# Performance work log

Measured on AMD Instinct MI355X. Metric: run time of the kernel, lower is better.

## Reference

```python
import jax, jax.numpy as jnp
import numpy as np

B_, T_, D_ = 2, 2048, 1024
DS_, EXPAND_ = 16, 2
DI_ = D_ * EXPAND_


def setup_inputs() -> dict:
    key = jax.random.key(0)
    ks = jax.random.split(key, 10)
    s = 0.02
    x = jax.random.normal(ks[0], (B_, T_, D_), jnp.float32)
    Win = jax.random.normal(ks[1], (2 * DI_, D_), jnp.float32) * s   # in_proj weight [2di, d]
    A_log = jax.random.uniform(ks[2], (DI_, DS_), jnp.float32, -4.0, -1.0)
    WB = jax.random.normal(ks[3], (DS_, D_), jnp.float32) * s        # B_proj
    WC = jax.random.normal(ks[4], (DS_, D_), jnp.float32) * s        # C_proj
    Wdt = jax.random.normal(ks[5], (DI_, D_), jnp.float32) * s       # dt_proj weight
    bdt = jnp.zeros((DI_,), jnp.float32)                              # dt_proj bias
    dt_bias = jnp.full((DI_,), -4.0, jnp.float32)
    gamma = jnp.ones((DI_,), jnp.float32)
    beta = jnp.zeros((DI_,), jnp.float32)
    Wout = jax.random.normal(ks[6], (D_, DI_), jnp.float32) * s      # out_proj
    return dict(x=x, Win=Win, A_log=A_log, WB=WB, WC=WC, Wdt=Wdt, bdt=bdt,
                dt_bias=dt_bias, gamma=gamma, beta=beta, Wout=Wout)


def _forward(x, Win, A_log, WB, WC, Wdt, bdt, dt_bias, gamma, beta, Wout):
    B, T, d = x.shape
    di, ds = A_log.shape
    xz = jnp.einsum('btd,ed->bte', x, Win)            # [B,T,2di]
    xi, z = xz[..., :di], xz[..., di:]
    z = jax.nn.silu(z)
    A = -jnp.exp(A_log)                                # [di,ds]
    Bm = jnp.einsum('btd,sd->bts', x, WB)              # [B,T,ds]
    C = jnp.einsum('btd,sd->bts', x, WC)               # [B,T,ds]
    dt = jax.nn.softplus(jnp.einsum('btd,ed->bte', x, Wdt) + bdt + dt_bias)  # [B,T,di]
    dtA = dt[..., None] * A                            # [B,T,di,ds]
    denom = 1.0 - dtA * 0.5
    A_bar = (1.0 + dtA * 0.5) / denom                  # bilinear (Tustin)
    B_bar = dt[..., None] / denom                      # [B,T,di,ds]

    def step(state, inp):
        Ab, Bb, Bt, xt, Ct = inp                       # [B,di,ds],[B,di,ds],[B,ds],[B,di],[B,ds]
        state = Ab * state + Bb * Bt[:, None, :] * xt[:, :, None]
        out = jnp.einsum('bds,bs->bd', state, Ct)
        return state, out

    tm = lambda a: jnp.swapaxes(a, 0, 1)               # time-major for scan
    state0 = jnp.zeros((B, di, ds), x.dtype)
    state, outs = jax.lax.scan(step, state0, (tm(A_bar), tm(B_bar), tm(Bm), tm(xi), tm(C)))
    out = jnp.swapaxes(outs, 0, 1) * z                 # [B,T,di]
    mu = out.mean(-1, keepdims=True)
    var = ((out - mu) ** 2).mean(-1, keepdims=True)
    normed = (out - mu) * jax.lax.rsqrt(var + 1e-5) * gamma + beta
    y = jnp.einsum('bte,de->btd', normed, Wout)
    return y, state


def reference(x, Win, A_log, WB, WC, Wdt, bdt, dt_bias, gamma, beta, Wout):
    return _forward(x, Win, A_log, WB, WC, Wdt, bdt, dt_bias, gamma, beta, Wout)
```

## Files before the change

### kernel.cpp

```cpp
#include <hip/hip_runtime.h>
#include <stdint.h>

#define B_ 2
#define T_ 2048
#define D_ 1024
#define DI_ 2048
#define DS_ 16
#define MROWS (B_*T_)
#define NC_ 32
#define CL_ (T_/NC_)
#define TT_ 32

typedef unsigned short u16;
typedef __attribute__((ext_vector_type(4))) float f32x4;
typedef __attribute__((ext_vector_type(8))) short short8;
typedef __attribute__((ext_vector_type(4))) unsigned short u16x4;

__device__ __forceinline__ float bf2f(u16 u) {
    union { uint32_t i; float f; } v; v.i = ((uint32_t)u) << 16; return v.f;
}
__device__ __forceinline__ u16 f2bf(float f) {
    union { float f; uint32_t i; } v; v.f = f;
    uint32_t r = v.i + 0x7fff + ((v.i >> 16) & 1);
    return (u16)(r >> 16);
}

__global__ __launch_bounds__(256) void cvt_kernel(const float* __restrict__ in,
                                                  u16* __restrict__ out, int n4) {
    int i = blockIdx.x * 256 + threadIdx.x;
    if (i < n4) {
        float4 v = ((const float4*)in)[i];
        u16x4 o;
        o.x = f2bf(v.x); o.y = f2bf(v.y); o.z = f2bf(v.z); o.w = f2bf(v.w);
        ((u16x4*)out)[i] = o;
    }
}

__global__ __launch_bounds__(256) void gemm_in(
    const u16* __restrict__ A, const u16* __restrict__ Win,
    const u16* __restrict__ Wdt,
    u16* __restrict__ xi, u16* __restrict__ z, u16* __restrict__ dtout,
    const float* __restrict__ b1, const float* __restrict__ b2) {
    __shared__ u16 lA[2][128 * 32];
    __shared__ u16 lB[2][128 * 32];
    const int K = D_;
    const int tid  = threadIdx.x;
    const int lane = tid & 63;
    const int wave = tid >> 6;
    const int wr = wave >> 1, wc = wave & 1;

    const int nwg = gridDim.x * gridDim.y;
    const int lin = blockIdx.y * gridDim.x + blockIdx.x;
    const int swz = (lin & 7) * (nwg >> 3) + (lin >> 3);
    const int bx = swz % gridDim.x, by = swz / gridDim.x;
    const int m0 = by * 128, n0 = bx * 128;
    const int region = n0 >> 11;
    const u16* W = (region < 2) ? (Win + (size_t)n0 * K)
                                : (Wdt + (size_t)(n0 - 4096) * K);

    f32x4 acc[4][4];
#pragma unroll
    for (int i = 0; i < 4; ++i)
#pragma unroll
        for (int j = 0; j < 4; ++j) acc[i][j] = (f32x4){0.f, 0.f, 0.f, 0.f};

    const int srow = tid >> 2;
    const int sseg = tid & 3;
    const int gseg = sseg ^ ((srow >> 1) & 3);

    const int fr = lane & 15, ks = lane >> 4;
    const int rsw = ks ^ ((fr >> 1) & 3);

    auto STAGE = [&](int buf, int k0) {
#pragma unroll
        for (int it = 0; it < 2; ++it) {
            int row = it * 64 + srow;
            const u16* sa = A + (size_t)(m0 + row) * K + k0 + gseg * 8;
            const u16* sw = W + (size_t)row * K + k0 + gseg * 8;
            __builtin_amdgcn_global_load_lds(
                (const __attribute__((address_space(1))) void*)sa,
                (__attribute__((address_space(3))) void*)(&lA[buf][row * 32 + sseg * 8]),
                16, 0, 0);
            __builtin_amdgcn_global_load_lds(
                (const __attribute__((address_space(1))) void*)sw,
                (__attribute__((address_space(3))) void*)(&lB[buf][row * 32 + sseg * 8]),
                16, 0, 0);
        }
    };

    STAGE(0, 0);
    __syncthreads();
    int cur = 0;
    for (int k0 = 0; k0 < K; k0 += 32) {
        if (k0 + 32 < K) STAGE(cur ^ 1, k0 + 32);
        short8 af[4], bfr[4];
#pragma unroll
        for (int i = 0; i < 4; ++i) {
            af[i]  = *(const short8*)(&lA[cur][(wr * 64 + i * 16 + fr) * 32 + rsw * 8]);
            bfr[i] = *(const short8*)(&lB[cur][(wc * 64 + i * 16 + fr) * 32 + rsw * 8]);
        }
#pragma unroll
        for (int i = 0; i < 4; ++i)
#pragma unroll
            for (int j = 0; j < 4; ++j)
                acc[i][j] = __builtin_amdgcn_mfma_f32_16x16x32_bf16(
                    af[i], bfr[j], acc[i][j], 0, 0, 0);
        __syncthreads();
        cur ^= 1;
    }

    const int fq = lane >> 4;
#pragma unroll
    for (int i = 0; i < 4; ++i)
#pragma unroll
        for (int j = 0; j < 4; ++j) {
            int gnl = n0 + wc * 64 + j * 16 + fr;
#pragma unroll
            for (int r = 0; r < 4; ++r) {
                int gm = m0 + wr * 64 + i * 16 + fq * 4 + r;
                float v = acc[i][j][r];
                if (region == 0) {
                    xi[(size_t)gm * DI_ + gnl] = f2bf(v);
                } else if (region == 1) {
                    v = v / (1.f + __expf(-v));
                    z[(size_t)gm * DI_ + (gnl - 2048)] = f2bf(v);
                } else {
                    int gn = gnl - 4096;
                    v += b1[gn] + b2[gn];
                    v = (v > 20.f) ? v : log1pf(__expf(v));
                    dtout[(size_t)gm * DI_ + gn] = f2bf(v);
                }
            }
        }
}

__global__ __launch_bounds__(256) void gemm_out(
    const u16* __restrict__ A, const u16* __restrict__ W,
    float* __restrict__ out, int M, int N, int K) {
    __shared__ u16 lA[2][128 * 32];
    __shared__ u16 lB[2][128 * 32];
    const int tid  = threadIdx.x;
    const int lane = tid & 63;
    const int wave = tid >> 6;
    const int wr = wave >> 1, wc = wave & 1;

    const int nwg = gridDim.x * gridDim.y;
    const int lin = blockIdx.y * gridDim.x + blockIdx.x;
    const int swz = (lin & 7) * (nwg >> 3) + (lin >> 3);
    const int bx = swz % gridDim.x, by = swz / gridDim.x;
    const int m0 = by * 128, n0 = bx * 128;

    f32x4 acc[4][4];
#pragma unroll
    for (int i = 0; i < 4; ++i)
#pragma unroll
        for (int j = 0; j < 4; ++j) acc[i][j] = (f32x4){0.f, 0.f, 0.f, 0.f};

    const int srow = tid >> 2;
    const int sseg = tid & 3;
    const int gseg = sseg ^ ((srow >> 1) & 3);
    const int fr = lane & 15, ks = lane >> 4;
    const int rsw = ks ^ ((fr >> 1) & 3);

    auto STAGE = [&](int buf, int k0) {
#pragma unroll
        for (int it = 0; it < 2; ++it) {
            int row = it * 64 + srow;
            const u16* sa = A + (size_t)(m0 + row) * K + k0 + gseg * 8;
            const u16* sw = W + (size_t)(n0 + row) * K + k0 + gseg * 8;
            __builtin_amdgcn_global_load_lds(
                (const __attribute__((address_space(1))) void*)sa,
                (__attribute__((address_space(3))) void*)(&lA[buf][row * 32 + sseg * 8]),
                16, 0, 0);
            __builtin_amdgcn_global_load_lds(
                (const __attribute__((address_space(1))) void*)sw,
                (__attribute__((address_space(3))) void*)(&lB[buf][row * 32 + sseg * 8]),
                16, 0, 0);
        }
    };

    STAGE(0, 0);
    __syncthreads();
    int cur = 0;
    for (int k0 = 0; k0 < K; k0 += 32) {
        if (k0 + 32 < K) STAGE(cur ^ 1, k0 + 32);
        short8 af[4], bfr[4];
#pragma unroll
        for (int i = 0; i < 4; ++i) {
            af[i]  = *(const short8*)(&lA[cur][(wr * 64 + i * 16 + fr) * 32 + rsw * 8]);
            bfr[i] = *(const short8*)(&lB[cur][(wc * 64 + i * 16 + fr) * 32 + rsw * 8]);
        }
#pragma unroll
        for (int i = 0; i < 4; ++i)
#pragma unroll
            for (int j = 0; j < 4; ++j)
                acc[i][j] = __builtin_amdgcn_mfma_f32_16x16x32_bf16(
                    af[i], bfr[j], acc[i][j], 0, 0, 0);
        __syncthreads();
        cur ^= 1;
    }

    const int fq = lane >> 4;
#pragma unroll
    for (int i = 0; i < 4; ++i)
#pragma unroll
        for (int j = 0; j < 4; ++j) {
            int gn = n0 + wc * 64 + j * 16 + fr;
#pragma unroll
            for (int r = 0; r < 4; ++r) {
                int gm = m0 + wr * 64 + i * 16 + fq * 4 + r;
                out[(size_t)gm * N + gn] = acc[i][j][r];
            }
        }
}

__global__ __launch_bounds__(256) void bc_kernel(
    const float* __restrict__ x, const float* __restrict__ WB,
    const float* __restrict__ WC, float* __restrict__ Bm, float* __restrict__ Cm) {
    __shared__ float xs[32][65];
    __shared__ float ws[32][65];
    int m0 = blockIdx.x * 32;
    int tid = threadIdx.x;
    int o = tid & 31, mg = tid >> 5;
    float acc[4] = {0.f, 0.f, 0.f, 0.f};
    for (int k0 = 0; k0 < D_; k0 += 64) {
        __syncthreads();
#pragma unroll
        for (int j = 0; j < 8; ++j) {
            int f = j * 256 + tid;
            int r = f >> 6, kk = f & 63;
            xs[r][kk] = x[(size_t)(m0 + r) * D_ + k0 + kk];
            ws[r][kk] = (r < 16) ? WB[(size_t)r * D_ + k0 + kk]
                                 : WC[(size_t)(r - 16) * D_ + k0 + kk];
        }
        __syncthreads();
#pragma unroll 8
        for (int kk = 0; kk < 64; ++kk) {
            float wv = ws[o][kk];
#pragma unroll
            for (int r = 0; r < 4; ++r)
                acc[r] = fmaf(xs[mg * 4 + r][kk], wv, acc[r]);
        }
    }
#pragma unroll
    for (int r = 0; r < 4; ++r) {
        int m = m0 + mg * 4 + r;
        if (o < 16) Bm[(size_t)m * DS_ + o] = acc[r];
        else        Cm[(size_t)m * DS_ + (o - 16)] = acc[r];
    }
}

__global__ __launch_bounds__(256) void scan1_kernel(
    const u16* __restrict__ dt, const u16* __restrict__ xi,
    const float* __restrict__ Bm, const float* __restrict__ A_log,
    float* __restrict__ P, float* __restrict__ Z) {
    const int c = blockIdx.x, dblk = blockIdx.y, b = blockIdx.z;
    const int tid = threadIdx.x;
    const int d = dblk * 256 + tid;
    __shared__ u16 sdt[TT_ * 256];
    __shared__ u16 sxi[TT_ * 256];
    __shared__ float sB[TT_ * 16];
    float A2[16], st[16], Pp[16];
#pragma unroll
    for (int s = 0; s < 16; ++s) {
        A2[s] = -0.5f * __expf(A_log[(size_t)d * DS_ + s]);
        st[s] = 0.f; Pp[s] = 1.f;
    }
    const size_t tb = (size_t)b * T_;
    for (int t0 = c * CL_; t0 < (c + 1) * CL_; t0 += TT_) {
        __syncthreads();
#pragma unroll
        for (int r = 0; r < 4; ++r) {
            int flat = r * 2048 + tid * 8;
            int row = flat >> 8, col = flat & 255;
            const u16* s1 = dt + (tb + t0 + row) * DI_ + dblk * 256 + col;
            const u16* s2 = xi + (tb + t0 + row) * DI_ + dblk * 256 + col;
            __builtin_amdgcn_global_load_lds(
                (const __attribute__((address_space(1))) void*)s1,
                (__attribute__((address_space(3))) void*)(sdt + flat), 16, 0, 0);
            __builtin_amdgcn_global_load_lds(
                (const __attribute__((address_space(1))) void*)s2,
                (__attribute__((address_space(3))) void*)(sxi + flat), 16, 0, 0);
        }
        *(float2*)(sB + tid * 2) = *(const float2*)(Bm + (tb + t0) * DS_ + tid * 2);
        __syncthreads();
#pragma unroll 2
        for (int tt = 0; tt < TT_; ++tt) {
            float dtv = bf2f(sdt[tt * 256 + tid]);
            float xiv = bf2f(sxi[tt * 256 + tid]);
            float dxv = dtv * xiv;
            float bv[16];
            *(float4*)&bv[0]  = *(const float4*)(sB + tt * 16);
            *(float4*)&bv[4]  = *(const float4*)(sB + tt * 16 + 4);
            *(float4*)&bv[8]  = *(const float4*)(sB + tt * 16 + 8);
            *(float4*)&bv[12] = *(const float4*)(sB + tt * 16 + 12);
#pragma unroll
            for (int s = 0; s < 16; ++s) {
                float a2   = fmaf(dtv, -A2[s], 1.f);
                float inv  = __builtin_amdgcn_rcpf(a2);
                float abar = fmaf(2.f, inv, -1.f);
                st[s] = fmaf(abar, st[s], (inv * bv[s]) * dxv);
                Pp[s] *= abar;
            }
        }
    }
    size_t base = (((size_t)b * DI_ + d) * NC_ + c) * 16;
#pragma unroll
    for (int q = 0; q < 4; ++q) {
        *(float4*)(P + base + q * 4) = (float4){Pp[q*4], Pp[q*4+1], Pp[q*4+2], Pp[q*4+3]};
        *(float4*)(Z + base + q * 4) = (float4){st[q*4], st[q*4+1], st[q*4+2], st[q*4+3]};
    }
}

__global__ __launch_bounds__(256) void scan2_kernel(
    float* __restrict__ P, const float* __restrict__ Z,
    float* __restrict__ st_out) {
    size_t idx = (size_t)blockIdx.x * 256 + threadIdx.x;
    size_t bd = idx >> 4;
    int s = (int)(idx & 15);
    float cur = 0.f;
    for (int c = 0; c < NC_; ++c) {
        size_t a = (bd * NC_ + c) * 16 + s;
        float p = P[a], zv = Z[a];
        P[a] = cur;
        cur = fmaf(p, cur, zv);
    }
    st_out[idx] = cur;
}

__global__ __launch_bounds__(256) void scan3_kernel(
    const u16* __restrict__ dt, const u16* __restrict__ xi,
    const float* __restrict__ Bm, const float* __restrict__ Cm,
    const float* __restrict__ A_log, const float* __restrict__ I,
    u16* __restrict__ so) {
    const int c = blockIdx.x, dblk = blockIdx.y, b = blockIdx.z;
    const int tid = threadIdx.x;
    const int d = dblk * 256 + tid;
    __shared__ u16 sdt[TT_ * 256];
    __shared__ u16 sxi[TT_ * 256];
    __shared__ float sB[TT_ * 16];
    __shared__ float sC[TT_ * 16];
    float A2[16], st[16];
#pragma unroll
    for (int s = 0; s < 16; ++s)
        A2[s] = -0.5f * __expf(A_log[(size_t)d * DS_ + s]);
    size_t base = (((size_t)b * DI_ + d) * NC_ + c) * 16;
#pragma unroll
    for (int q = 0; q < 4; ++q) {
        float4 v = *(const float4*)(I + base + q * 4);
        st[q*4] = v.x; st[q*4+1] = v.y; st[q*4+2] = v.z; st[q*4+3] = v.w;
    }
    const size_t tb = (size_t)b * T_;
    for (int t0 = c * CL_; t0 < (c + 1) * CL_; t0 += TT_) {
        __syncthreads();
#pragma unroll
        for (int r = 0; r < 4; ++r) {
            int flat = r * 2048 + tid * 8;
            int row = flat >> 8, col = flat & 255;
            const u16* s1 = dt + (tb + t0 + row) * DI_ + dblk * 256 + col;
            const u16* s2 = xi + (tb + t0 + row) * DI_ + dblk * 256 + col;
            __builtin_amdgcn_global_load_lds(
                (const __attribute__((address_space(1))) void*)s1,
                (__attribute__((address_space(3))) void*)(sdt + flat), 16, 0, 0);
            __builtin_amdgcn_global_load_lds(
                (const __attribute__((address_space(1))) void*)s2,
                (__attribute__((address_space(3))) void*)(sxi + flat), 16, 0, 0);
        }
        *(float2*)(sB + tid * 2) = *(const float2*)(Bm + (tb + t0) * DS_ + tid * 2);
        *(float2*)(sC + tid * 2) = *(const float2*)(Cm + (tb + t0) * DS_ + tid * 2);
        __syncthreads();
#pragma unroll 2
        for (int tt = 0; tt < TT_; ++tt) {
            float dtv = bf2f(sdt[tt * 256 + tid]);
            float xiv = bf2f(sxi[tt * 256 + tid]);
            float dxv = dtv * xiv;
            float bv[16], cv[16];
            *(float4*)&bv[0]  = *(const float4*)(sB + tt * 16);
            *(float4*)&bv[4]  = *(const float4*)(sB + tt * 16 + 4);
            *(float4*)&bv[8]  = *(const float4*)(sB + tt * 16 + 8);
            *(float4*)&bv[12] = *(const float4*)(sB + tt * 16 + 12);
            *(float4*)&cv[0]  = *(const float4*)(sC + tt * 16);
            *(float4*)&cv[4]  = *(const float4*)(sC + tt * 16 + 4);
            *(float4*)&cv[8]  = *(const float4*)(sC + tt * 16 + 8);
            *(float4*)&cv[12] = *(const float4*)(sC + tt * 16 + 12);
            float acc = 0.f;
#pragma unroll
            for (int s = 0; s < 16; ++s) {
                float a2   = fmaf(dtv, -A2[s], 1.f);
                float inv  = __builtin_amdgcn_rcpf(a2);
                float abar = fmaf(2.f, inv, -1.f);
                st[s] = fmaf(abar, st[s], (inv * bv[s]) * dxv);
                acc = fmaf(st[s], cv[s], acc);
            }
            so[(tb + t0 + tt) * DI_ + d] = f2bf(acc);
        }
    }
}

__global__ __launch_bounds__(256) void ln_kernel(
    const u16* __restrict__ so, const u16* __restrict__ z,
    const float* __restrict__ gamma, const float* __restrict__ beta,
    u16* __restrict__ normed) {
    int m = blockIdx.x;
    int tid = threadIdx.x;
    size_t base = (size_t)m * DI_;
    float v[8];
    float s = 0.f, s2 = 0.f;
#pragma unroll
    for (int j = 0; j < 8; ++j) {
        int i = tid + j * 256;
        float val = bf2f(so[base + i]) * bf2f(z[base + i]);
        v[j] = val; s += val; s2 += val * val;
    }
#pragma unroll
    for (int off = 32; off; off >>= 1) {
        s  += __shfl_xor(s,  off);
        s2 += __shfl_xor(s2, off);
    }
    __shared__ float rs[4], rq[4];
    int wave = tid >> 6;
    if ((tid & 63) == 0) { rs[wave] = s; rq[wave] = s2; }
    __syncthreads();
    s  = rs[0] + rs[1] + rs[2] + rs[3];
    s2 = rq[0] + rq[1] + rq[2] + rq[3];
    float mu  = s * (1.f / DI_);
    float var = s2 * (1.f / DI_) - mu * mu;
    float rstd = rsqrtf(var + 1e-5f);
#pragma unroll
    for (int j = 0; j < 8; ++j) {
        int i = tid + j * 256;
        float nv = (v[j] - mu) * rstd * gamma[i] + beta[i];
        normed[base + i] = f2bf(nv);
    }
}

extern "C" void kernel_launch(void* const* d_in, const int* in_sizes, int n_in,
                              void* d_out, int out_size, void* d_ws, size_t ws_size,
                              hipStream_t stream) {
    const float* x       = (const float*)d_in[0];
    const float* Win     = (const float*)d_in[1];
    const float* A_log   = (const float*)d_in[2];
    const float* WB      = (const float*)d_in[3];
    const float* WC      = (const float*)d_in[4];
    const float* Wdt     = (const float*)d_in[5];
    const float* bdt     = (const float*)d_in[6];
    const float* dt_bias = (const float*)d_in[7];
    const float* gamma   = (const float*)d_in[8];
    const float* beta    = (const float*)d_in[9];
    const float* Wout    = (const float*)d_in[10];

    float* y_out     = (float*)d_out;
    float* state_out = y_out + (size_t)B_ * T_ * D_;

    char* ws = (char*)d_ws;
    u16* xi_bf   = (u16*)(ws + 0);
    u16* z_bf    = (u16*)(ws + 16777216);
    u16* dt_bf   = (u16*)(ws + 33554432);
    u16* so_bf   = (u16*)(ws + 50331648);
    u16* nm_bf   = (u16*)(ws + 67108864);
    u16* x_bf    = (u16*)(ws + 83886080);
    u16* win_bf  = (u16*)(ws + 92274688);
    u16* wdt_bf  = (u16*)(ws + 100663296);
    u16* wout_bf = (u16*)(ws + 104857600);
    float* BmB   = (float*)(ws + 109051904);
    float* CmB   = (float*)(ws + 109314048);

    float* Pc = (float*)(ws + 83886080);
    float* Zc = (float*)(ws + 92274688);

    {
        int n4;
        n4 = (B_ * T_ * D_) / 4;
        cvt_kernel<<<(n4 + 255) / 256, 256, 0, stream>>>(x, x_bf, n4);
        n4 = (2 * DI_ * D_) / 4;
        cvt_kernel<<<(n4 + 255) / 256, 256, 0, stream>>>(Win, win_bf, n4);
        n4 = (DI_ * D_) / 4;
        cvt_kernel<<<(n4 + 255) / 256, 256, 0, stream>>>(Wdt, wdt_bf, n4);
        n4 = (D_ * DI_) / 4;
        cvt_kernel<<<(n4 + 255) / 256, 256, 0, stream>>>(Wout, wout_bf, n4);
    }

    dim3 blk(256);
    gemm_in<<<dim3(6144 / 128, MROWS / 128), blk, 0, stream>>>(
        x_bf, win_bf, wdt_bf, xi_bf, z_bf, dt_bf, bdt, dt_bias);
    bc_kernel<<<MROWS / 32, 256, 0, stream>>>(x, WB, WC, BmB, CmB);

    scan1_kernel<<<dim3(NC_, DI_ / 256, B_), blk, 0, stream>>>(
        dt_bf, xi_bf, BmB, A_log, Pc, Zc);
    scan2_kernel<<<(B_ * DI_ * DS_) / 256, blk, 0, stream>>>(
        Pc, Zc, state_out);
    scan3_kernel<<<dim3(NC_, DI_ / 256, B_), blk, 0, stream>>>(
        dt_bf, xi_bf, BmB, CmB, A_log, Pc, so_bf);

    ln_kernel<<<MROWS, 256, 0, stream>>>(so_bf, z_bf, gamma, beta, nm_bf);
    gemm_out<<<dim3(D_ / 128, MROWS / 128), blk, 0, stream>>>(
        nm_bf, wout_bf, y_out, MROWS, D_, DI_);
}
```

Measured before the change: 415.6 us.

## Triple-buffer GEMM LDS staging with explicit vmcnt waits and drop block swizzle

Both GEMM kernels move from double to triple LDS buffers. Two tiles are kept in flight, with explicit s_waitcnt vmcnt counts and raw s_barrier calls replacing the __syncthreads-per-iteration loop. The goal is to hide global-to-LDS load latency behind MFMA work. The change also removes the L2-locality block-index swizzle and uses plain blockIdx mapping, which may reduce cache reuse. LDS use per block grows from 32KB to 48KB, which may lower occupancy.

```diff
diff --git a/kernel.cpp b/kernel.cpp
--- a/kernel.cpp
+++ b/kernel.cpp
@@ -41,19 +41,15 @@
     const u16* __restrict__ Wdt,
     u16* __restrict__ xi, u16* __restrict__ z, u16* __restrict__ dtout,
     const float* __restrict__ b1, const float* __restrict__ b2) {
-    __shared__ u16 lA[2][128 * 32];
-    __shared__ u16 lB[2][128 * 32];
+    __shared__ u16 lA[3][128 * 32];
+    __shared__ u16 lB[3][128 * 32];
     const int K = D_;
+    const int NK = K / 32;
     const int tid  = threadIdx.x;
     const int lane = tid & 63;
     const int wave = tid >> 6;
     const int wr = wave >> 1, wc = wave & 1;
-
-    const int nwg = gridDim.x * gridDim.y;
-    const int lin = blockIdx.y * gridDim.x + blockIdx.x;
-    const int swz = (lin & 7) * (nwg >> 3) + (lin >> 3);
-    const int bx = swz % gridDim.x, by = swz / gridDim.x;
-    const int m0 = by * 128, n0 = bx * 128;
+    const int m0 = blockIdx.y * 128, n0 = blockIdx.x * 128;
     const int region = n0 >> 11;
     const u16* W = (region < 2) ? (Win + (size_t)n0 * K)
                                 : (Wdt + (size_t)(n0 - 4096) * K);
@@ -67,7 +63,6 @@
     const int srow = tid >> 2;
     const int sseg = tid & 3;
     const int gseg = sseg ^ ((srow >> 1) & 3);
-
     const int fr = lane & 15, ks = lane >> 4;
     const int rsw = ks ^ ((fr >> 1) & 3);
 
@@ -87,17 +82,12 @@
                 16, 0, 0);
         }
     };
-
-    STAGE(0, 0);
-    __syncthreads();
-    int cur = 0;
-    for (int k0 = 0; k0 < K; k0 += 32) {
-        if (k0 + 32 < K) STAGE(cur ^ 1, k0 + 32);
+    auto COMPUTE = [&](int buf) {
         short8 af[4], bfr[4];
 #pragma unroll
         for (int i = 0; i < 4; ++i) {
-            af[i]  = *(const short8*)(&lA[cur][(wr * 64 + i * 16 + fr) * 32 + rsw * 8]);
-            bfr[i] = *(const short8*)(&lB[cur][(wc * 64 + i * 16 + fr) * 32 + rsw * 8]);
+            af[i]  = *(const short8*)(&lA[buf][(wr * 64 + i * 16 + fr) * 32 + rsw * 8]);
+            bfr[i] = *(const short8*)(&lB[buf][(wc * 64 + i * 16 + fr) * 32 + rsw * 8]);
         }
 #pragma unroll
         for (int i = 0; i < 4; ++i)
@@ -105,9 +95,35 @@
             for (int j = 0; j < 4; ++j)
                 acc[i][j] = __builtin_amdgcn_mfma_f32_16x16x32_bf16(
                     af[i], bfr[j], acc[i][j], 0, 0, 0);
-        __syncthreads();
-        cur ^= 1;
-    }
+    };
+
+    STAGE(0, 0); STAGE(1, 32); STAGE(2, 64);
+    asm volatile("s_waitcnt vmcnt(8)" ::: "memory");
+    __builtin_amdgcn_s_barrier();
+    __builtin_amdgcn_sched_barrier(0);
+
+    int cur = 0;
+    for (int k = 0; k < NK - 3; ++k) {
+        COMPUTE(cur);
+        __builtin_amdgcn_s_barrier();
+        __builtin_amdgcn_sched_barrier(0);
+        STAGE(cur, (k + 3) * 32);
+        asm volatile("s_waitcnt vmcnt(8)" ::: "memory");
+        __builtin_amdgcn_s_barrier();
+        __builtin_amdgcn_sched_barrier(0);
+        cur = (cur == 2) ? 0 : cur + 1;
+    }
+    COMPUTE(cur);
+    asm volatile("s_waitcnt vmcnt(4)" ::: "memory");
+    __builtin_amdgcn_s_barrier();
+    __builtin_amdgcn_sched_barrier(0);
+    cur = (cur == 2) ? 0 : cur + 1;
+    COMPUTE(cur);
+    asm volatile("s_waitcnt vmcnt(0)" ::: "memory");
+    __builtin_amdgcn_s_barrier();
+    __builtin_amdgcn_sched_barrier(0);
+    cur = (cur == 2) ? 0 : cur + 1;
+    COMPUTE(cur);
 
     const int fq = lane >> 4;
 #pragma unroll
@@ -137,18 +153,14 @@
 __global__ __launch_bounds__(256) void gemm_out(
     const u16* __restrict__ A, const u16* __restrict__ W,
     float* __restrict__ out, int M, int N, int K) {
-    __shared__ u16 lA[2][128 * 32];
-    __shared__ u16 lB[2][128 * 32];
+    __shared__ u16 lA[3][128 * 32];
+    __shared__ u16 lB[3][128 * 32];
+    const int NK = K / 32;
     const int tid  = threadIdx.x;
     const int lane = tid & 63;
     const int wave = tid >> 6;
     const int wr = wave >> 1, wc = wave & 1;
-
-    const int nwg = gridDim.x * gridDim.y;
-    const int lin = blockIdx.y * gridDim.x + blockIdx.x;
-    const int swz = (lin & 7) * (nwg >> 3) + (lin >> 3);
-    const int bx = swz % gridDim.x, by = swz / gridDim.x;
-    const int m0 = by * 128, n0 = bx * 128;
+    const int m0 = blockIdx.y * 128, n0 = blockIdx.x * 128;
 
     f32x4 acc[4][4];
 #pragma unroll
@@ -178,17 +190,12 @@
                 16, 0, 0);
         }
     };
-
-    STAGE(0, 0);
-    __syncthreads();
-    int cur = 0;
-    for (int k0 = 0; k0 < K; k0 += 32) {
-        if (k0 + 32 < K) STAGE(cur ^ 1, k0 + 32);
+    auto COMPUTE = [&](int buf) {
         short8 af[4], bfr[4];
 #pragma unroll
         for (int i = 0; i < 4; ++i) {
-            af[i]  = *(const short8*)(&lA[cur][(wr * 64 + i * 16 + fr) * 32 + rsw * 8]);
-            bfr[i] = *(const short8*)(&lB[cur][(wc * 64 + i * 16 + fr) * 32 + rsw * 8]);
+            af[i]  = *(const short8*)(&lA[buf][(wr * 64 + i * 16 + fr) * 32 + rsw * 8]);
+            bfr[i] = *(const short8*)(&lB[buf][(wc * 64 + i * 16 + fr) * 32 + rsw * 8]);
         }
 #pragma unroll
         for (int i = 0; i < 4; ++i)
@@ -196,9 +203,35 @@
             for (int j = 0; j < 4; ++j)
                 acc[i][j] = __builtin_amdgcn_mfma_f32_16x16x32_bf16(
                     af[i], bfr[j], acc[i][j], 0, 0, 0);
-        __syncthreads();
-        cur ^= 1;
-    }
+    };
+
+    STAGE(0, 0); STAGE(1, 32); STAGE(2, 64);
+    asm volatile("s_waitcnt vmcnt(8)" ::: "memory");
+    __builtin_amdgcn_s_barrier();
+    __builtin_amdgcn_sched_barrier(0);
+
+    int cur = 0;
+    for (int k = 0; k < NK - 3; ++k) {
+        COMPUTE(cur);
+        __builtin_amdgcn_s_barrier();
+        __builtin_amdgcn_sched_barrier(0);
+        STAGE(cur, (k + 3) * 32);
+        asm volatile("s_waitcnt vmcnt(8)" ::: "memory");
+        __builtin_amdgcn_s_barrier();
+        __builtin_amdgcn_sched_barrier(0);
+        cur = (cur == 2) ? 0 : cur + 1;
+    }
+    COMPUTE(cur);
+    asm volatile("s_waitcnt vmcnt(4)" ::: "memory");
+    __builtin_amdgcn_s_barrier();
+    __builtin_amdgcn_sched_barrier(0);
+    cur = (cur == 2) ? 0 : cur + 1;
+    COMPUTE(cur);
+    asm volatile("s_waitcnt vmcnt(0)" ::: "memory");
+    __builtin_amdgcn_s_barrier();
+    __builtin_amdgcn_sched_barrier(0);
+    cur = (cur == 2) ? 0 : cur + 1;
+    COMPUTE(cur);
 
     const int fq = lane >> 4;
 #pragma unroll
```

Result: slower. 425.3 us (+2.3%).

## Deepen input GEMM pipeline to four LDS stages and drop block swizzle

Applied to the files above, without the earlier changes.

The input-projection GEMM moves from a double-buffered loop with two full __syncthreads per K step to a 4-buffer ring that keeps three tiles in flight. It waits with explicit vmcnt counts and a single s_barrier, and raises wave priority around the MFMA block. The point is to hide global-to-LDS load latency behind matrix math. Both GEMMs also drop the XCD/L2 block-index swizzle in favour of plain row-major block mapping, which may hurt cache locality. LDS use doubles, which could lower occupancy, and correctness of the ring reuse depends on the hand-counted vmcnt values.

```diff
diff --git a/kernel.cpp b/kernel.cpp
--- a/kernel.cpp
+++ b/kernel.cpp
@@ -41,19 +41,15 @@
     const u16* __restrict__ Wdt,
     u16* __restrict__ xi, u16* __restrict__ z, u16* __restrict__ dtout,
     const float* __restrict__ b1, const float* __restrict__ b2) {
-    __shared__ u16 lA[2][128 * 32];
-    __shared__ u16 lB[2][128 * 32];
+    __shared__ u16 lA[4][128 * 32];
+    __shared__ u16 lB[4][128 * 32];
     const int K = D_;
+    const int NSUB = K / 32;
     const int tid  = threadIdx.x;
     const int lane = tid & 63;
     const int wave = tid >> 6;
     const int wr = wave >> 1, wc = wave & 1;
-
-    const int nwg = gridDim.x * gridDim.y;
-    const int lin = blockIdx.y * gridDim.x + blockIdx.x;
-    const int swz = (lin & 7) * (nwg >> 3) + (lin >> 3);
-    const int bx = swz % gridDim.x, by = swz / gridDim.x;
-    const int m0 = by * 128, n0 = bx * 128;
+    const int m0 = blockIdx.y * 128, n0 = blockIdx.x * 128;
     const int region = n0 >> 11;
     const u16* W = (region < 2) ? (Win + (size_t)n0 * K)
                                 : (Wdt + (size_t)(n0 - 4096) * K);
@@ -67,11 +63,11 @@
     const int srow = tid >> 2;
     const int sseg = tid & 3;
     const int gseg = sseg ^ ((srow >> 1) & 3);
-
     const int fr = lane & 15, ks = lane >> 4;
     const int rsw = ks ^ ((fr >> 1) & 3);
 
-    auto STAGE = [&](int buf, int k0) {
+    auto STAGE = [&](int buf, int t) {
+        const int k0 = t * 32;
 #pragma unroll
         for (int it = 0; it < 2; ++it) {
             int row = it * 64 + srow;
@@ -87,27 +83,44 @@
                 16, 0, 0);
         }
     };
-
-    STAGE(0, 0);
-    __syncthreads();
-    int cur = 0;
-    for (int k0 = 0; k0 < K; k0 += 32) {
-        if (k0 + 32 < K) STAGE(cur ^ 1, k0 + 32);
+    auto COMPUTE = [&](int buf) {
         short8 af[4], bfr[4];
 #pragma unroll
         for (int i = 0; i < 4; ++i) {
-            af[i]  = *(const short8*)(&lA[cur][(wr * 64 + i * 16 + fr) * 32 + rsw * 8]);
-            bfr[i] = *(const short8*)(&lB[cur][(wc * 64 + i * 16 + fr) * 32 + rsw * 8]);
-        }
+            af[i]  = *(const short8*)(&lA[buf][(wr * 64 + i * 16 + fr) * 32 + rsw * 8]);
+            bfr[i] = *(const short8*)(&lB[buf][(wc * 64 + i * 16 + fr) * 32 + rsw * 8]);
+        }
+        __builtin_amdgcn_s_setprio(1);
 #pragma unroll
         for (int i = 0; i < 4; ++i)
 #pragma unroll
             for (int j = 0; j < 4; ++j)
                 acc[i][j] = __builtin_amdgcn_mfma_f32_16x16x32_bf16(
                     af[i], bfr[j], acc[i][j], 0, 0, 0);
-        __syncthreads();
-        cur ^= 1;
-    }
+        __builtin_amdgcn_s_setprio(0);
+    };
+
+    STAGE(0, 0); STAGE(1, 1); STAGE(2, 2);
+    asm volatile("s_waitcnt vmcnt(8)" ::: "memory");
+    __builtin_amdgcn_s_barrier();
+    asm volatile("" ::: "memory");
+
+    for (int t = 0; t < NSUB - 3; ++t) {
+        STAGE((t + 3) & 3, t + 3);
+        COMPUTE(t & 3);
+        asm volatile("s_waitcnt vmcnt(8)" ::: "memory");
+        __builtin_amdgcn_s_barrier();
+        asm volatile("" ::: "memory");
+    }
+    COMPUTE((NSUB - 3) & 3);
+    asm volatile("s_waitcnt vmcnt(4)" ::: "memory");
+    __builtin_amdgcn_s_barrier();
+    asm volatile("" ::: "memory");
+    COMPUTE((NSUB - 2) & 3);
+    asm volatile("s_waitcnt vmcnt(0)" ::: "memory");
+    __builtin_amdgcn_s_barrier();
+    asm volatile("" ::: "memory");
+    COMPUTE((NSUB - 1) & 3);
 
     const int fq = lane >> 4;
 #pragma unroll
@@ -143,12 +156,7 @@
     const int lane = tid & 63;
     const int wave = tid >> 6;
     const int wr = wave >> 1, wc = wave & 1;
-
-    const int nwg = gridDim.x * gridDim.y;
-    const int lin = blockIdx.y * gridDim.x + blockIdx.x;
-    const int swz = (lin & 7) * (nwg >> 3) + (lin >> 3);
-    const int bx = swz % gridDim.x, by = swz / gridDim.x;
-    const int m0 = by * 128, n0 = bx * 128;
+    const int m0 = blockIdx.y * 128, n0 = blockIdx.x * 128;
 
     f32x4 acc[4][4];
 #pragma unroll
```

After: 434.1 us. 4.5% more time.
